# Kernel optimization log

Hardware: AMD Instinct MI355X
Metric: run time of the kernel (lower is better)

The kernel has to match this reference:

```python
import jax, jax.numpy as jnp
import numpy as np

B, S, D = 8, 2048, 1024

def setup_inputs() -> dict:
    key = jax.random.key(0)
    ks = jax.random.split(key, 7)
    x = jax.random.normal(ks[0], (B, S, D), dtype=jnp.float32)
    s = 1.0 / np.sqrt(D)
    Wq = jax.random.normal(ks[1], (D, D), dtype=jnp.float32) * s
    bq = jax.random.normal(ks[2], (D,), dtype=jnp.float32) * 0.01
    Wk = jax.random.normal(ks[3], (D, D), dtype=jnp.float32) * s
    bk = jax.random.normal(ks[4], (D,), dtype=jnp.float32) * 0.01
    Wv = jax.random.normal(ks[5], (D, D), dtype=jnp.float32) * s
    bv = jax.random.normal(ks[6], (D,), dtype=jnp.float32) * 0.01
    return {"x": x, "Wq": Wq, "bq": bq, "Wk": Wk, "bk": bk, "Wv": Wv, "bv": bv}

def reference(x, Wq, bq, Wk, bk, Wv, bv):
    # QKV projections: [B,S,D]
    Q = jnp.einsum('bsd,de->bse', x, Wq) + bq
    K = jnp.einsum('bsd,de->bse', x, Wk) + bk
    V = jnp.einsum('bsd,de->bse', x, Wv) + bv
    scale = 1.0 / jnp.sqrt(jnp.asarray(Q.shape[-1], Q.dtype))
    attn = jnp.einsum('bqd,bkd->bqk', Q, K) * scale  # [B,S,S]
    attn = jax.nn.softmax(attn, axis=-1)
    return jnp.einsum('bqk,bkd->bqd', attn, V)
```

## Files before the change

### kernel.cpp

```cpp
#include <hip/hip_runtime.h>
#include <cstdint>


#define Bb 8
#define Ss 2048
#define Dd 1024

typedef unsigned short ushort_t;
typedef __attribute__((ext_vector_type(8))) short short8;
typedef __attribute__((ext_vector_type(4))) float floatx4;

__device__ inline ushort_t f2bf(float f) {
    unsigned int u = __float_as_uint(f);
    unsigned int r = (u + 0x7fffu + ((u >> 16) & 1u)) >> 16;
    return (ushort_t)r;
}
__device__ inline float bf2f(ushort_t u) {
    return __uint_as_float(((unsigned int)u) << 16);
}

__device__ inline floatx4 mfma16(short8 a, short8 b, floatx4 c) {
    return __builtin_amdgcn_mfma_f32_16x16x32_bf16(a, b, c, 0, 0, 0);
}

__device__ inline void gload16(const void* g, void* l) {
    __builtin_amdgcn_global_load_lds(
        (const __attribute__((address_space(1))) void*)g,
        (__attribute__((address_space(3))) void*)l, 16, 0, 0);
}

__device__ __attribute__((always_inline)) void gemm_core256(
    const ushort_t* __restrict__ A, const ushort_t* __restrict__ B,
    int K, int lda, int ldb, int m0, int n0, int tid,
    ushort_t* lds, floatx4 acc[8][4])
{
    const int lane = tid & 63;
    const int wave = tid >> 6;
    const int l3   = lane >> 3;
    const int kc   = ((lane & 7) ^ l3) * 8;

    const ushort_t* aS[2][2];
    const ushort_t* bS[2][2];
#pragma unroll
    for (int i = 0; i < 2; i++) {
#pragma unroll
        for (int g = 0; g < 2; g++) {
            const int r = i * 128 + g * 64 + wave * 8 + l3;
            aS[g][i] = A + (size_t)(m0 + r) * lda + kc;
        }
#pragma unroll
        for (int nh = 0; nh < 2; nh++) {
            const int c = wave + i * 8;
            const int r = (c >> 2) * 64 + nh * 32 + (c & 3) * 8 + l3;
            bS[nh][i] = B + (size_t)(n0 + r) * ldb + kc;
        }
    }

    const int jA   = (wave >> 2) * 64 + (lane & 15);
    const int jB   = (wave & 3) * 32 + (lane & 15);
    const int swz0 = (((lane >> 4) + 0) ^ (lane & 7)) * 8;
    const int swz1 = (((lane >> 4) + 4) ^ (lane & 7)) * 8;

    short8 bFr[4][2];
    short8 aE[2][2], aO[2][2];

#define STG(DST, REGI, SRC, KOFS)                                             \
    do {                                                                      \
        gload16(SRC[0] + (KOFS), (DST) + (REGI) * 8192 + wave * 512);         \
        gload16(SRC[1] + (KOFS), (DST) + (REGI) * 8192 + (wave + 8) * 512);   \
    } while (0)

#define RD_B_ALL(BUF)                                                         \
    _Pragma("unroll")                                                         \
    for (int nf = 0; nf < 4; nf++) {                                          \
        const ushort_t* pB_ =                                                 \
            (BUF) + (2 + (nf >> 1)) * 8192 + (jB + (nf & 1) * 16) * 64;       \
        bFr[nf][0] = *(const short8*)&pB_[swz0];                              \
        bFr[nf][1] = *(const short8*)&pB_[swz1];                              \
    }

#define RD_A(BUF, Q, DST)                                                     \
    _Pragma("unroll")                                                         \
    for (int mi = 0; mi < 2; mi++) {                                          \
        const ushort_t* pA_ = (BUF) + ((Q) >> 1) * 8192 +                     \
                              (jA + ((Q) & 1) * 32 + mi * 16) * 64;           \
        DST[mi][0] = *(const short8*)&pA_[swz0];                              \
        DST[mi][1] = *(const short8*)&pA_[swz1];                              \
    }

#define MM(Q, ASRC)                                                           \
    _Pragma("unroll")                                                         \
    for (int ks = 0; ks < 2; ks++)                                            \
        _Pragma("unroll")                                                     \
        for (int mi = 0; mi < 2; mi++)                                        \
            _Pragma("unroll")                                                 \
            for (int nf = 0; nf < 4; nf++)                                    \
                acc[(Q) * 2 + mi][nf] =                                       \
                    mfma16(ASRC[mi][ks], bFr[nf][ks], acc[(Q) * 2 + mi][nf]);

#define MMPH(Q, ASRC)                                                         \
    do {                                                                      \
        asm volatile("s_waitcnt lgkmcnt(0)" ::: "memory");                    \
        __builtin_amdgcn_sched_barrier(0);                                    \
        __builtin_amdgcn_s_setprio(1);                                        \
        MM(Q, ASRC);                                                          \
        __builtin_amdgcn_s_setprio(0);                                        \
        __builtin_amdgcn_sched_barrier(0);                                    \
    } while (0)

    STG(lds, 0, aS[0], 0);
    STG(lds, 1, aS[1], 0);
    STG(lds, 2, bS[0], 0);
    STG(lds, 3, bS[1], 0);
    STG(lds + 32768, 2, bS[0], 64);
    STG(lds + 32768, 3, bS[1], 64);
    asm volatile("s_waitcnt vmcnt(4)" ::: "memory");
    __builtin_amdgcn_s_barrier();
    __builtin_amdgcn_sched_barrier(0);

    const int NT = K >> 6;
    for (int t = 0; t < NT; t++) {
        const ushort_t* cb = lds + (t & 1) * 32768;
        ushort_t* nb = lds + ((t + 1) & 1) * 32768;
        ushort_t* sb = lds + (t & 1) * 32768;
        const int k1 = (t + 1 < NT ? t + 1 : 0) << 6;
        const int k2 = (t + 2 < NT ? t + 2 : 0) << 6;

        RD_B_ALL(cb);
        RD_A(cb, 0, aE);

        MMPH(0, aE);
        RD_A(cb, 1, aO);
        STG(nb, 0, aS[0], k1);
        MMPH(1, aO);
        RD_A(cb, 2, aE);
        STG(nb, 1, aS[1], k1);
        __builtin_amdgcn_sched_barrier(0);
        __builtin_amdgcn_s_barrier();
        __builtin_amdgcn_sched_barrier(0);
        MMPH(2, aE);
        RD_A(cb, 3, aO);
        STG(sb, 2, bS[0], k2);
        MMPH(3, aO);
        STG(sb, 3, bS[1], k2);
        __builtin_amdgcn_sched_barrier(0);
        asm volatile("s_waitcnt vmcnt(4)" ::: "memory");
        __builtin_amdgcn_s_barrier();
        __builtin_amdgcn_sched_barrier(0);
    }
    asm volatile("s_waitcnt vmcnt(0)" ::: "memory");
#undef MMPH
#undef MM
#undef RD_A
#undef RD_B_ALL
#undef STG
}

template <int EPI>
__global__ __launch_bounds__(512, 2) void gemm256(
    const ushort_t* __restrict__ A, const ushort_t* __restrict__ B,
    void* __restrict__ Cv, float* __restrict__ aux,
    int K, int lda, int ldb, int ldc,
    size_t strideA, size_t strideB, size_t strideC)
{
    const int z = blockIdx.z;
    A += (size_t)z * strideA;
    B += (size_t)z * strideB;
    const int m0 = blockIdx.y * 256;
    const int n0 = blockIdx.x * 256;

    __shared__ __align__(16) ushort_t lds[2 * 4 * 8192];

    floatx4 acc[8][4] = {};
    gemm_core256(A, B, K, lda, ldb, m0, n0, (int)threadIdx.x, lds, acc);

    const int lane = threadIdx.x & 63;
    const int wave = threadIdx.x >> 6;
    const int row0 = m0 + (wave >> 2) * 128 + (lane >> 4) * 4;
    const int col0 = n0 + (wave & 3) * 64 + (lane & 15);

    if (EPI == 0) {
        ushort_t* Cb = (ushort_t*)Cv;
        float bval[4];
#pragma unroll
        for (int nf = 0; nf < 4; nf++) bval[nf] = aux[col0 + nf * 16];
#pragma unroll
        for (int mf = 0; mf < 8; mf++)
#pragma unroll
            for (int i = 0; i < 4; i++) {
                const size_t ro = (size_t)(row0 + mf * 16 + i) * ldc;
#pragma unroll
                for (int nf = 0; nf < 4; nf++)
                    Cb[ro + col0 + nf * 16] = f2bf(acc[mf][nf][i] + bval[nf]);
            }
    } else if (EPI == 1) {
        ushort_t* Cb = (ushort_t*)Cv + (size_t)z * strideC;
        float* ls = aux + z * Ss;
        float rs[8][4];
#pragma unroll
        for (int mf = 0; mf < 8; mf++)
#pragma unroll
            for (int i = 0; i < 4; i++) rs[mf][i] = 0.f;
#pragma unroll
        for (int mf = 0; mf < 8; mf++)
#pragma unroll
            for (int i = 0; i < 4; i++) {
                const size_t ro = (size_t)(row0 + mf * 16 + i) * ldc;
#pragma unroll
                for (int nf = 0; nf < 4; nf++) {
                    const ushort_t o = f2bf(__expf(acc[mf][nf][i] * 0.03125f));
                    Cb[ro + col0 + nf * 16] = o;
                    rs[mf][i] += bf2f(o);
                }
            }
#pragma unroll
        for (int mf = 0; mf < 8; mf++)
#pragma unroll
            for (int i = 0; i < 4; i++) {
                float s = rs[mf][i];
                s += __shfl_xor(s, 1);
                s += __shfl_xor(s, 2);
                s += __shfl_xor(s, 4);
                s += __shfl_xor(s, 8);
                rs[mf][i] = s;
            }
        if ((lane & 15) == 0) {
#pragma unroll
            for (int mf = 0; mf < 8; mf++)
#pragma unroll
                for (int i = 0; i < 4; i++)
                    atomicAdd(&ls[row0 + mf * 16 + i], rs[mf][i]);
        }
    } else {
        float* Cf = (float*)Cv + (size_t)z * strideC;
#pragma unroll
        for (int mf = 0; mf < 8; mf++)
#pragma unroll
            for (int i = 0; i < 4; i++) {
                const int gr = row0 + mf * 16 + i;
                const float iv = 1.0f / aux[z * Ss + gr];
#pragma unroll
                for (int nf = 0; nf < 4; nf++)
                    Cf[(size_t)gr * ldc + col0 + nf * 16] = acc[mf][nf][i] * iv;
            }
    }
}

__global__ __launch_bounds__(256) void vtrans(
    const ushort_t* __restrict__ QKVb, ushort_t* __restrict__ Vt)
{
    __shared__ __align__(16) ushort_t tile[64][72];
    const int t = blockIdx.x;
    const int z = t >> 9, rem = t & 511;
    const int d0 = (rem & 15) * 64, s0 = (rem >> 4) * 64;
    const int tid = threadIdx.x;
    const int rr = tid >> 3;
    const int c8 = (tid & 7) * 8;
#pragma unroll
    for (int i = 0; i < 2; i++) {
        const int s = s0 + rr + i * 32;
        uint4 v = *(const uint4*)&QKVb[((size_t)(z * Ss + s)) * 3072 + 2048 + d0 + c8];
        *(uint4*)&tile[rr + i * 32][c8] = v;
    }
    __syncthreads();
#pragma unroll
    for (int i = 0; i < 2; i++) {
        const int d = rr + i * 32;
        ushort_t u[8];
#pragma unroll
        for (int j = 0; j < 8; j++) u[j] = tile[c8 + j][d];
        *(uint4*)&Vt[(size_t)z * Dd * Ss + (size_t)(d0 + d) * Ss + s0 + c8] =
            *(const uint4*)u;
    }
}

__global__ __launch_bounds__(256) void prep(
    const float* __restrict__ x,
    const float* __restrict__ W0, const float* __restrict__ W1,
    const float* __restrict__ W2,
    const float* __restrict__ bq, const float* __restrict__ bk,
    const float* __restrict__ bv,
    ushort_t* __restrict__ xb, ushort_t* __restrict__ Wall,
    float* __restrict__ ball)
{
    const int bid = blockIdx.x;
    const int tid = threadIdx.x;

    if (bid < 8192) {
        const size_t i = (size_t)bid * 256 + tid;
        const float4* p = (const float4*)x + i * 2;
        float4 a = p[0], b = p[1];
        ushort_t u[8];
        u[0]=f2bf(a.x); u[1]=f2bf(a.y); u[2]=f2bf(a.z); u[3]=f2bf(a.w);
        u[4]=f2bf(b.x); u[5]=f2bf(b.y); u[6]=f2bf(b.z); u[7]=f2bf(b.w);
        *(uint4*)(xb + i * 8) = *(const uint4*)u;
    } else if (bid < 8960) {
        const int t = bid - 8192;
        const int z = t >> 8;
        const float* W = (z == 0) ? W0 : (z == 1) ? W1 : W2;
        ushort_t* Wt = Wall + (size_t)z * Dd * Dd;
        __shared__ float tt[64][65];
        const int n0 = ((t >> 4) & 15) * 64, k0 = (t & 15) * 64;
        const int r  = tid >> 4;
        const int c4 = (tid & 15) * 4;
#pragma unroll
        for (int i = 0; i < 4; i++) {
            float4 v = *(const float4*)&W[(size_t)(k0 + r + i * 16) * Dd + n0 + c4];
            tt[r + i * 16][c4 + 0] = v.x;
            tt[r + i * 16][c4 + 1] = v.y;
            tt[r + i * 16][c4 + 2] = v.z;
            tt[r + i * 16][c4 + 3] = v.w;
        }
        __syncthreads();
#pragma unroll
        for (int i = 0; i < 4; i++) {
            const int rn = r + i * 16;
            ushort_t u[4];
#pragma unroll
            for (int j = 0; j < 4; j++) u[j] = f2bf(tt[c4 + j][rn]);
            *(uint2*)&Wt[(size_t)(n0 + rn) * Dd + k0 + c4] = *(const uint2*)u;
        }
    } else {
#pragma unroll
        for (int j = 0; j < 12; j++) {
            const int idx = j * 256 + tid;
            float v = (idx < 1024) ? bq[idx]
                    : (idx < 2048) ? bk[idx - 1024] : bv[idx - 2048];
            ball[idx] = v;
        }
    }
}

extern "C" void kernel_launch(void* const* d_in, const int* in_sizes, int n_in,
                              void* d_out, int out_size, void* d_ws, size_t ws_size,
                              hipStream_t stream)
{
    const float* x  = (const float*)d_in[0];
    const float* Wq = (const float*)d_in[1];
    const float* bq = (const float*)d_in[2];
    const float* Wk = (const float*)d_in[3];
    const float* bk = (const float*)d_in[4];
    const float* Wv = (const float*)d_in[5];
    const float* bv = (const float*)d_in[6];
    float* out = (float*)d_out;

    char* ws = (char*)d_ws;
    const size_t MB = 1u << 20;
    ushort_t* xb   = (ushort_t*)(ws);
    ushort_t* Vt   = (ushort_t*)(ws);
    ushort_t* QKVb = (ushort_t*)(ws + 32 * MB);
    ushort_t* Pb   = (ushort_t*)(ws + 128 * MB);
    float*    lsum = (float*)(ws + 192 * MB);
    ushort_t* Wall = (ushort_t*)d_out;
    float*    ball = (float*)((char*)d_out + 6 * MB);

    prep<<<8961, 256, 0, stream>>>(x, Wq, Wk, Wv, bq, bk, bv, xb, Wall, ball);

    dim3 g1(3072 / 256, 16384 / 256, 1);
    gemm256<0><<<g1, 512, 0, stream>>>(xb, Wall, QKVb, ball,
                                       Dd, Dd, Dd, 3072, 0, 0, 0);

    hipMemsetAsync(lsum, 0, (size_t)Bb * Ss * sizeof(float), stream);
    vtrans<<<4096, 256, 0, stream>>>(QKVb, Vt);
    dim3 g2(Ss / 256, Ss / 256, Bb);
    gemm256<1><<<g2, 512, 0, stream>>>(QKVb, QKVb + 1024, Pb, lsum,
                                       Dd, 3072, 3072, Ss,
                                       (size_t)Ss * 3072, (size_t)Ss * 3072,
                                       (size_t)Ss * Ss);

    dim3 g3(Dd / 256, Ss / 256, Bb);
    gemm256<3><<<g3, 512, 0, stream>>>(Pb, Vt, out, lsum,
                                       Ss, Ss, Ss, Dd,
                                       (size_t)Ss * Ss, (size_t)Dd * Ss,
                                       (size_t)Ss * Dd);
}
```

Baseline: 372.4 us.

## Prefetch next tile's A/B LDS fragments during last MFMA phase

Moves the LDS reads of the next K-tile's B fragments and first A fragment out of the top of the loop. They are now issued during the final MFMA phase of the previous iteration, and the first tile is preloaded before the loop. The waitcnt thresholds and barrier placement are changed so the MFMAs overlap with these LDS reads. This is meant to hide LDS read latency at iteration boundaries. The tighter vmcnt and lgkmcnt accounting risks hazards or extra stalls, and it depends on the STG into the same buffer being ordered correctly.

```diff
diff --git a/kernel.cpp b/kernel.cpp
--- a/kernel.cpp
+++ b/kernel.cpp
@@ -98,13 +98,20 @@
                 acc[(Q) * 2 + mi][nf] =                                       \
                     mfma16(ASRC[mi][ks], bFr[nf][ks], acc[(Q) * 2 + mi][nf]);
 
-#define MMPH(Q, ASRC)                                                         \
+#define MMPH(Q, ASRC, WN)                                                     \
     do {                                                                      \
-        asm volatile("s_waitcnt lgkmcnt(0)" ::: "memory");                    \
+        asm volatile("s_waitcnt lgkmcnt(" #WN ")" ::: "memory");              \
         __builtin_amdgcn_sched_barrier(0);                                    \
         __builtin_amdgcn_s_setprio(1);                                        \
         MM(Q, ASRC);                                                          \
         __builtin_amdgcn_s_setprio(0);                                        \
+        __builtin_amdgcn_sched_barrier(0);                                    \
+    } while (0)
+
+#define SBAR()                                                                \
+    do {                                                                      \
+        __builtin_amdgcn_sched_barrier(0);                                    \
+        __builtin_amdgcn_s_barrier();                                         \
         __builtin_amdgcn_sched_barrier(0);                                    \
     } while (0)
 
@@ -117,6 +124,8 @@
     asm volatile("s_waitcnt vmcnt(4)" ::: "memory");
     __builtin_amdgcn_s_barrier();
     __builtin_amdgcn_sched_barrier(0);
+    RD_B_ALL(lds);
+    RD_A(lds, 0, aE);
 
     const int NT = K >> 6;
     for (int t = 0; t < NT; t++) {
@@ -126,29 +135,27 @@
         const int k1 = (t + 1 < NT ? t + 1 : 0) << 6;
         const int k2 = (t + 2 < NT ? t + 2 : 0) << 6;
 
-        RD_B_ALL(cb);
-        RD_A(cb, 0, aE);
-
-        MMPH(0, aE);
+        MMPH(0, aE, 0);
         RD_A(cb, 1, aO);
         STG(nb, 0, aS[0], k1);
-        MMPH(1, aO);
+        MMPH(1, aO, 0);
         RD_A(cb, 2, aE);
         STG(nb, 1, aS[1], k1);
-        __builtin_amdgcn_sched_barrier(0);
-        __builtin_amdgcn_s_barrier();
-        __builtin_amdgcn_sched_barrier(0);
-        MMPH(2, aE);
+        SBAR();
+        MMPH(2, aE, 0);
         RD_A(cb, 3, aO);
         STG(sb, 2, bS[0], k2);
-        MMPH(3, aO);
+        __builtin_amdgcn_sched_barrier(0);
+        asm volatile("s_waitcnt vmcnt(2)" ::: "memory");
+        SBAR();
+        RD_A(nb, 0, aE);
+        MMPH(3, aO, 4);
+        RD_B_ALL(nb);
         STG(sb, 3, bS[1], k2);
-        __builtin_amdgcn_sched_barrier(0);
-        asm volatile("s_waitcnt vmcnt(4)" ::: "memory");
-        __builtin_amdgcn_s_barrier();
-        __builtin_amdgcn_sched_barrier(0);
+        SBAR();
     }
     asm volatile("s_waitcnt vmcnt(0)" ::: "memory");
+#undef SBAR
 #undef MMPH
 #undef MM
 #undef RD_A
```

Result: slower. 387.6 us (+4.1%).
